# Kernel tuning notes

Measured on AMD Instinct MI355X. Metric: run time of the kernel, lower is better.

## Reference

```python
import jax, jax.numpy as jnp
import numpy as np

N = 2048          # num atoms
ATOM_D = 64       # atom embedding dim
H = 8             # num heads
NB = 8            # num bond types
D = ATOM_D * H    # 512, Q/K/V output dim
NEG_SLOPE = 0.2


def setup_inputs() -> dict:
    key = jax.random.key(0)
    ks = jax.random.split(key, 12)
    inp = {
        "atom_embeddings": jax.random.normal(ks[0], (N, ATOM_D), dtype=jnp.float32),
        # bond type per (i, j); -1 means no bond (masked)
        "edges": jax.random.randint(ks[1], (N, N), -1, NB, dtype=jnp.int32),
        "Qw": jax.random.normal(ks[2], (ATOM_D, D), dtype=jnp.float32) / np.sqrt(ATOM_D),
        "Qb": jnp.zeros((D,), dtype=jnp.float32),
        "Kw": jax.random.normal(ks[3], (ATOM_D, D), dtype=jnp.float32) / np.sqrt(ATOM_D),
        "Kb": jnp.zeros((D,), dtype=jnp.float32),
        "Vw": jax.random.normal(ks[4], (ATOM_D, D), dtype=jnp.float32) / np.sqrt(ATOM_D),
        "Vb": jnp.zeros((D,), dtype=jnp.float32),
        # per-bond-type attention weights: (NB, 2*D, H), xavier-ish scale
        "a": jax.random.normal(ks[5], (NB, 2 * D, H), dtype=jnp.float32) * np.sqrt(2.0 / (2 * D + H)) * 1.414,
        "Pw": jax.random.normal(ks[6], (D, ATOM_D), dtype=jnp.float32) / np.sqrt(D),
        "Pb": jnp.zeros((ATOM_D,), dtype=jnp.float32),
    }
    return inp


def reference(atom_embeddings, edges, Qw, Qb, Kw, Kb, Vw, Vb, a, Pw, Pb):
    n, d = atom_embeddings.shape
    nb, two_d, h = a.shape
    D_ = two_d // 2
    Q = atom_embeddings @ Qw + Qb          # (N, D)
    K = atom_embeddings @ Kw + Kb          # (N, D)
    V = atom_embeddings @ Vw + Vb          # (N, D)

    # a[k] applies to concat(Q_i, K_j): split into src / dst halves
    A1 = a[:, :D_, :]                      # (NB, D, H)
    A2 = a[:, D_:, :]                      # (NB, D, H)
    # precompute per-node, per-bond-type partial scores (avoids the dense
    # one-hot scatter of the original: direct per-edge-type weight indexing)
    S1 = jnp.einsum('id,kdh->ikh', Q, A1)  # (N, NB, H)
    S2 = jnp.einsum('jd,kdh->jkh', K, A2)  # (N, NB, H)

    kidx = jnp.clip(edges, 0, nb - 1)      # (N, N)
    rows = jnp.arange(n)
    # e[i,j,h] = S1[i, edges[i,j], h] + S2[j, edges[i,j], h]
    e = S1[rows[:, None], kidx] + S2[rows[None, :], kidx]   # (N, N, H)
    valid = (edges >= 0)[..., None]
    # masked edges get all-zero rows in the original scatter -> score exactly 0
    e = jnp.where(valid, jax.nn.leaky_relu(e, negative_slope=NEG_SLOPE), 0.0)

    attn = jax.nn.softmax(e, axis=1)       # softmax over neighbor j
    Vh = V.reshape(n, h, d)                # (N, H, atom_d)
    out = jnp.einsum('ijh,jhd->ihd', attn, Vh).reshape(n, h * d)
    return out @ Pw + Pb                   # (N, atom_d)
```

## Files before the change

kernel.cpp:

```cpp
#include <hip/hip_runtime.h>

#define NN 2048
#define AD 64
#define HH 8
#define DD 512
#define NEG 0.2f

typedef float f32x4 __attribute__((ext_vector_type(4)));
typedef _Float16 half8 __attribute__((ext_vector_type(8)));
typedef _Float16 half2v __attribute__((ext_vector_type(2)));
typedef unsigned short u16;
typedef unsigned int u32;
typedef u16 u16x8 __attribute__((ext_vector_type(8)));

__global__ __launch_bounds__(256) void prep_vth_kernel(
    const float* __restrict__ Qw, const float* __restrict__ Qb,
    const float* __restrict__ Kw, const float* __restrict__ Kb,
    const float* __restrict__ A,
    const float* __restrict__ X,
    const float* __restrict__ Vw, const float* __restrict__ Vb,
    float* __restrict__ W1, float* __restrict__ W2, float* __restrict__ c12,
    u16* __restrict__ VtH) {
  __shared__ float As[512][8];
  __shared__ float Ws8[8][516];
  __shared__ float red[4][8][8];
  __shared__ float red2[8][8];
  __shared__ float Xs[64][68];
  int t = threadIdx.x;
  int b = blockIdx.x;
  if (b < 128) {
    int mat = b >> 6;
    int k = (b >> 3) & 7;
    int dg = b & 7;
    int d0 = dg * 8;
    const float* Asrc = A + (size_t)k * 8192 + mat * 4096;
    const float* Wsrc = (mat ? Kw : Qw) + (size_t)d0 * DD;

    float* Asf = &As[0][0];
    for (int idx = t; idx < 4096; idx += 256) Asf[idx] = Asrc[idx];
    for (int idx = t; idx < 4096; idx += 256) {
      int dd = idx >> 9, c = idx & 511;
      Ws8[dd][c] = Wsrc[idx];
    }
    __syncthreads();

    int dd = t & 7, h = (t >> 3) & 7, cs = t >> 6;
    int cbase = cs * 128;
    float acc = 0.f;
#pragma unroll 4
    for (int c = 0; c < 128; ++c) {
      acc += Ws8[dd][cbase + c] * As[cbase + c][h];
    }
    red[cs][dd][h] = acc;
    __syncthreads();
    if (t < 64) {
      int dd2 = t >> 3, h2 = t & 7;
      float v = red[0][dd2][h2] + red[1][dd2][h2] + red[2][dd2][h2] + red[3][dd2][h2];
      (mat ? W2 : W1)[(d0 + dd2) * 64 + k * 8 + h2] = v;
    }
    if (dg == 0) {
      if (t < 64) {
        int h2 = t >> 3, seg = t & 7;
        const float* bs = mat ? Kb : Qb;
        float a2 = 0.f;
        for (int i = 0; i < 64; ++i) {
          int c = seg * 64 + i;
          a2 += bs[c] * As[c][h2];
        }
        red2[h2][seg] = a2;
      }
      __syncthreads();
      if (t < 8) {
        float s = 0.f;
#pragma unroll
        for (int seg = 0; seg < 8; ++seg) s += red2[t][seg];
        c12[mat * 64 + k * 8 + t] = s;
      }
    }
  } else {
    int tile = b - 128;
    int r0 = (tile >> 2) * 64;
    int d0 = (tile & 3) * 128;

    for (int idx = t; idx < 64 * 64; idx += 256) {
      int r = idx >> 6, c = idx & 63;
      Xs[r][c] = X[(size_t)(r0 + r) * AD + c];
    }
    __syncthreads();

    int tr = t >> 5;
    int td = t & 31;
    int d = d0 + td * 4;
    float4 bias = *(const float4*)&Vb[d];
    float4 acc[8];
#pragma unroll
    for (int i = 0; i < 8; ++i) acc[i] = bias;
    for (int c = 0; c < 64; ++c) {
      float4 w = *(const float4*)&Vw[c * DD + d];
#pragma unroll
      for (int i = 0; i < 8; ++i) {
        float x = Xs[tr * 8 + i][c];
        acc[i].x += x * w.x; acc[i].y += x * w.y;
        acc[i].z += x * w.z; acc[i].w += x * w.w;
      }
    }
#pragma unroll
    for (int c = 0; c < 4; ++c) {
      u16x8 o;
#pragma unroll
      for (int i = 0; i < 8; ++i) {
        float fv = (c == 0) ? acc[i].x : (c == 1) ? acc[i].y
                 : (c == 2) ? acc[i].z : acc[i].w;
        _Float16 hf = (_Float16)fv;
        o[i] = __builtin_bit_cast(u16, hf);
      }
      *(u16x8*)&VtH[(size_t)(d + c) * NN + r0 + tr * 8] = o;
    }
  }
}

__global__ __launch_bounds__(256) void stab_kernel(
    const float* __restrict__ X,
    const float* __restrict__ W1, const float* __restrict__ W2,
    const float* __restrict__ c12,
    u16* __restrict__ TS1, u16* __restrict__ TS2) {
  __shared__ float W1L[64][65];
  __shared__ float W2L[64][65];
  __shared__ float XS[16][65];
  __shared__ __align__(16) u16 T1S[16][128];
  __shared__ __align__(16) u16 T2S[16][128];
  int t = threadIdx.x;
  int r0 = blockIdx.x * 16;
  for (int i = t; i < 4096; i += 256) {
    int d = i >> 6, kh = i & 63;
    W1L[d][kh] = W1[i];
    W2L[d][kh] = W2[i];
  }
  {
    int r = t >> 4, c = (t & 15) * 4;
    float4 xv = *(const float4*)&X[(size_t)(r0 + r) * AD + c];
    XS[r][c] = xv.x; XS[r][c + 1] = xv.y; XS[r][c + 2] = xv.z; XS[r][c + 3] = xv.w;
  }
  __syncthreads();
  int r = t >> 4, khq = t & 15;
  float a1[4], a2[4];
#pragma unroll
  for (int i = 0; i < 4; ++i) {
    a1[i] = c12[khq * 4 + i];
    a2[i] = c12[64 + khq * 4 + i];
  }
  for (int d = 0; d < 64; ++d) {
    float x = XS[r][d];
#pragma unroll
    for (int i = 0; i < 4; ++i) {
      a1[i] += x * W1L[d][khq * 4 + i];
      a2[i] += x * W2L[d][khq * 4 + i];
    }
  }
#pragma unroll
  for (int i = 0; i < 4; ++i) {
    int kh = khq * 4 + i, k = kh >> 3, h = kh & 7;
    int kki = (k ^ (r & 7)) << 4;
    _Float16 p1 = (_Float16)(__expf(a1[i]) * 0.25f);
    _Float16 n1 = (_Float16)(__expf(NEG * a1[i]) * 0.25f);
    _Float16 p2 = (_Float16)(__expf(a2[i]) * 0.25f);
    _Float16 n2 = (_Float16)(__expf(NEG * a2[i]) * 0.25f);
    T1S[r][kki + h]     = __builtin_bit_cast(u16, p1);
    T1S[r][kki + 8 + h] = __builtin_bit_cast(u16, n1);
    T2S[r][kki + h]     = __builtin_bit_cast(u16, p2);
    T2S[r][kki + 8 + h] = __builtin_bit_cast(u16, n2);
  }
  __syncthreads();
  {
    const u16* s1 = &T1S[0][0];
    const u16* s2 = &T2S[0][0];
    *(u16x8*)&TS1[(size_t)r0 * 128 + t * 8] = *(const u16x8*)&s1[t * 8];
    *(u16x8*)&TS2[(size_t)r0 * 128 + t * 8] = *(const u16x8*)&s2[t * 8];
  }
}

__global__ __launch_bounds__(512, 4) void attn_mfma_kernel(
    const int* __restrict__ E,
    const u16* __restrict__ TS1, const u16* __restrict__ TS2,
    const u16* __restrict__ VtH,
    float* __restrict__ PART, float* __restrict__ LPART) {
  __shared__ _Float16 s1t[16 * 128];
  __shared__ _Float16 s2t[2][64 * 128];
  __shared__ _Float16 PA[2][8][16][72];
  int t = threadIdx.x;
  int w = t >> 6, lane = t & 63;
  int li = lane & 15, q = lane >> 4;
  int m = lane & 31;
  int i_loc = w * 2 + (lane >> 5);
  int it = blockIdx.x >> 1, ch = blockIdx.x & 1;
  int i0 = it * 16, jch = ch * 1024;

  const half8 SIX8 = {(_Float16)0.0625f, (_Float16)0.0625f, (_Float16)0.0625f,
                      (_Float16)0.0625f, (_Float16)0.0625f, (_Float16)0.0625f,
                      (_Float16)0.0625f, (_Float16)0.0625f};
  const half8 ONE8 = {(_Float16)1.0f, (_Float16)1.0f, (_Float16)1.0f,
                      (_Float16)1.0f, (_Float16)1.0f, (_Float16)1.0f,
                      (_Float16)1.0f, (_Float16)1.0f};

  if (t < 256) {
    *(u16x8*)&s1t[t * 8] = *(const u16x8*)&TS1[(size_t)i0 * 128 + t * 8];
  }
  {
    const u16* src = TS2 + (size_t)jch * 128;
    *(u16x8*)&s2t[0][t * 8]        = *(const u16x8*)&src[t * 8];
    *(u16x8*)&s2t[0][4096 + t * 8] = *(const u16x8*)&src[4096 + t * 8];
  }
  u16x8 stA = *(const u16x8*)&TS2[(size_t)(jch + 64) * 128 + t * 8];
  u16x8 stB = *(const u16x8*)&TS2[(size_t)(jch + 64) * 128 + 4096 + t * 8];
  const int* Erow = E + (size_t)(i0 + i_loc) * NN;
  int2 eCur = *(const int2*)(Erow + jch + 2 * m);
  int2 eNxt = *(const int2*)(Erow + jch + 64 + 2 * m);
  __syncthreads();

  f32x4 acc[4];
#pragma unroll
  for (int n = 0; n < 4; ++n) acc[n] = (f32x4){0.f, 0.f, 0.f, 0.f};
  f32x4 acc_l = (f32x4){0.f, 0.f, 0.f, 0.f};
  int cur = 0;

#pragma unroll 1
  for (int jt = 0; jt < 16; ++jt) {
    int jb = jch + jt * 64;

    u16x8 stA2, stB2;
    int2 eN2 = eNxt;
    if (jt < 14) {
      const u16* src = TS2 + (size_t)(jb + 128) * 128;
      stA2 = *(const u16x8*)&src[t * 8];
      stB2 = *(const u16x8*)&src[4096 + t * 8];
      eN2 = *(const int2*)(Erow + jb + 128 + 2 * m);
    }

    half8 bfrag[4][2];
#pragma unroll
    for (int n = 0; n < 4; ++n)
#pragma unroll
      for (int s = 0; s < 2; ++s) {
        const u16* p = &VtH[(size_t)(w * 64 + n * 16 + li) * NN + jb + s * 32 + q * 8];
        bfrag[n][s] = *(const half8*)p;
      }

    const _Float16* s1row = &s1t[i_loc * 128];
    const _Float16* s2row = &s2t[cur][0];
    half8 pmj[2];
#pragma unroll
    for (int jj = 0; jj < 2; ++jj) {
      int ev = jj ? eCur.y : eCur.x;
      int j = 2 * m + jj;
      int k = min(max(ev, 0), 7);
      int kki = (k ^ (i_loc & 7)) << 4;
      int kkj = (k ^ (j & 7)) << 4;
      half8 ip = *(const half8*)&s1row[kki];
      half8 in_ = *(const half8*)&s1row[kki + 8];
      half8 jp = *(const half8*)&s2row[j * 128 + kkj];
      half8 jn = *(const half8*)&s2row[j * 128 + kkj + 8];
      half8 pp = ip * jp;
      half8 pn = in_ * jn;
      half8 pm = __builtin_elementwise_max(pp, pn);
      if (ev < 0) pm = SIX8;
      pmj[jj] = pm;
    }
#pragma unroll
    for (int h = 0; h < 8; ++h) {
      half2v wv = {pmj[0][h], pmj[1][h]};
      *(half2v*)&PA[cur][h][i_loc][2 * m] = wv;
    }

    if (jt < 15) {
      *(u16x8*)&s2t[cur ^ 1][t * 8]        = stA;
      *(u16x8*)&s2t[cur ^ 1][4096 + t * 8] = stB;
    }

    asm volatile("s_waitcnt lgkmcnt(0)" ::: "memory");
    __builtin_amdgcn_s_barrier();

    half8 af0 = *(const half8*)&PA[cur][w][li][q * 8];
    half8 af1 = *(const half8*)&PA[cur][w][li][32 + q * 8];
    __builtin_amdgcn_s_setprio(1);
#pragma unroll
    for (int n = 0; n < 4; ++n) {
      acc[n] = __builtin_amdgcn_mfma_f32_16x16x32_f16(af0, bfrag[n][0], acc[n], 0, 0, 0);
      acc[n] = __builtin_amdgcn_mfma_f32_16x16x32_f16(af1, bfrag[n][1], acc[n], 0, 0, 0);
    }
    acc_l = __builtin_amdgcn_mfma_f32_16x16x32_f16(af0, ONE8, acc_l, 0, 0, 0);
    acc_l = __builtin_amdgcn_mfma_f32_16x16x32_f16(af1, ONE8, acc_l, 0, 0, 0);
    __builtin_amdgcn_s_setprio(0);

    stA = stA2; stB = stB2;
    eCur = eNxt; eNxt = eN2;
    cur ^= 1;
  }

  if (li == 0) {
#pragma unroll
    for (int r = 0; r < 4; ++r)
      LPART[((size_t)ch * NN + i0 + q * 4 + r) * 8 + w] = acc_l[r];
  }

  float* base = PART + (size_t)ch * NN * DD;
#pragma unroll
  for (int n = 0; n < 4; ++n) {
#pragma unroll
    for (int r = 0; r < 4; ++r) {
      int row = i0 + q * 4 + r;
      int col = w * 64 + n * 16 + li;
      base[(size_t)row * DD + col] = acc[n][r];
    }
  }
}

__global__ __launch_bounds__(256) void proj_kernel(
    const float* __restrict__ PART, const float* __restrict__ LPART,
    const float* __restrict__ Pw, const float* __restrict__ Pb,
    float* __restrict__ out) {
  __shared__ __align__(16) float preS[4][512];
  __shared__ float linv[4][8];
  int t = threadIdx.x;
  int r0 = blockIdx.x * 4;
  if (t < 32) {
    int i = t >> 3, h = t & 7;
    float s = 0.f;
#pragma unroll
    for (int c = 0; c < 2; ++c)
      s += LPART[(size_t)c * NN * 8 + (size_t)(r0 + i) * 8 + h];
    linv[i][h] = 1.0f / s;
  }
  __syncthreads();
  for (int idx = t; idx < 4 * 128; idx += 256) {
    int i = idx >> 7, hd = (idx & 127) * 4;
    float4 v = {0.f, 0.f, 0.f, 0.f};
#pragma unroll
    for (int c = 0; c < 2; ++c) {
      float4 p = *(const float4*)&PART[(size_t)c * NN * DD + (size_t)(r0 + i) * DD + hd];
      v.x += p.x; v.y += p.y; v.z += p.z; v.w += p.w;
    }
    float li2 = linv[i][hd >> 6];
    v.x *= li2; v.y *= li2; v.z *= li2; v.w *= li2;
    *(float4*)&preS[i][hd] = v;
  }
  __syncthreads();
  int c = t & 63, rq = t >> 6;
  float acc0 = Pb[c];
  for (int hq = 0; hq < 128; ++hq) {
    int hd = hq * 4;
    float4 p0 = *(const float4*)&preS[rq][hd];
    float w0 = Pw[(hd + 0) * 64 + c];
    float w1 = Pw[(hd + 1) * 64 + c];
    float w2 = Pw[(hd + 2) * 64 + c];
    float w3 = Pw[(hd + 3) * 64 + c];
    acc0 += p0.x * w0 + p0.y * w1 + p0.z * w2 + p0.w * w3;
  }
  out[(size_t)(r0 + rq) * 64 + c] = acc0;
}

extern "C" void kernel_launch(void* const* d_in, const int* in_sizes, int n_in,
                              void* d_out, int out_size, void* d_ws, size_t ws_size,
                              hipStream_t stream) {
  const float* X  = (const float*)d_in[0];
  const int*   E  = (const int*)d_in[1];
  const float* Qw = (const float*)d_in[2];
  const float* Qb = (const float*)d_in[3];
  const float* Kw = (const float*)d_in[4];
  const float* Kb = (const float*)d_in[5];
  const float* Vw = (const float*)d_in[6];
  const float* Vb = (const float*)d_in[7];
  const float* A  = (const float*)d_in[8];
  const float* Pw = (const float*)d_in[9];
  const float* Pb = (const float*)d_in[10];
  float* out = (float*)d_out;

  float* ws = (float*)d_ws;
  const size_t ND = (size_t)NN * DD;
  float* PART  = ws;
  u16*   TS1   = (u16*)(ws + 2 * ND);
  u16*   TS2   = TS1 + (size_t)NN * 128;
  u16*   VtH   = TS2 + (size_t)NN * 128;
  float* LPART = (float*)(VtH + (size_t)DD * NN);
  float* W1    = LPART + (size_t)2 * NN * 8;
  float* W2    = W1 + 4096;
  float* c12   = W2 + 4096;

  prep_vth_kernel<<<256, 256, 0, stream>>>(Qw, Qb, Kw, Kb, A, X, Vw, Vb,
                                           W1, W2, c12, VtH);
  stab_kernel<<<128, 256, 0, stream>>>(X, W1, W2, c12, TS1, TS2);
  attn_mfma_kernel<<<256, 512, 0, stream>>>(E, TS1, TS2, VtH, PART, LPART);
  proj_kernel<<<512, 256, 0, stream>>>(PART, LPART, Pw, Pb, out);
}
```

Measured before the change: 66.92 us.

## Fuse four kernels into one cooperative kernel with grid-wide syncs

Merges the prep/V-projection, score-table, attention MFMA and output-projection kernels into a single cooperative launch of 256 blocks of 512 threads, separated by grid.sync() barriers. Each phase's thread mapping is adapted to 512 threads and shared memory is carved from one buffer. This removes three kernel launch boundaries and their drain/fill gaps. In exchange, grid barriers add their own cost, the projection phase now runs on half as many blocks, and the attention phase drops from four to two blocks per CU by launch bounds.

```diff
diff --git a/kernel.cpp b/kernel.cpp
--- a/kernel.cpp
+++ b/kernel.cpp
@@ -1,4 +1,7 @@
 #include <hip/hip_runtime.h>
+#include <hip/hip_cooperative_groups.h>
+
+namespace cg = cooperative_groups;
 
 #define NN 2048
 #define AD 64
@@ -12,22 +15,24 @@
 typedef unsigned short u16;
 typedef unsigned int u32;
 typedef u16 u16x8 __attribute__((ext_vector_type(8)));
-
-__global__ __launch_bounds__(256) void prep_vth_kernel(
+typedef u16 u16x4 __attribute__((ext_vector_type(4)));
+
+__global__ __launch_bounds__(512, 2) void fused_kernel(
     const float* __restrict__ Qw, const float* __restrict__ Qb,
     const float* __restrict__ Kw, const float* __restrict__ Kb,
-    const float* __restrict__ A,
-    const float* __restrict__ X,
+    const float* __restrict__ A,  const float* __restrict__ X,
     const float* __restrict__ Vw, const float* __restrict__ Vb,
+    const int* __restrict__ E,
+    const float* __restrict__ Pw, const float* __restrict__ Pb,
     float* __restrict__ W1, float* __restrict__ W2, float* __restrict__ c12,
-    u16* __restrict__ VtH) {
-  __shared__ float As[512][8];
-  __shared__ float Ws8[8][516];
-  __shared__ float red[4][8][8];
-  __shared__ float red2[8][8];
-  __shared__ float Xs[64][68];
+    u16* __restrict__ VtH, u16* __restrict__ TS1, u16* __restrict__ TS2,
+    float* __restrict__ PART, float* __restrict__ LPART,
+    float* __restrict__ out) {
+  __shared__ __align__(16) char smem[73728];
+  cg::grid_group grid = cg::this_grid();
   int t = threadIdx.x;
   int b = blockIdx.x;
+
   if (b < 128) {
     int mat = b >> 6;
     int k = (b >> 3) & 7;
@@ -35,327 +40,314 @@
     int d0 = dg * 8;
     const float* Asrc = A + (size_t)k * 8192 + mat * 4096;
     const float* Wsrc = (mat ? Kw : Qw) + (size_t)d0 * DD;
-
-    float* Asf = &As[0][0];
-    for (int idx = t; idx < 4096; idx += 256) Asf[idx] = Asrc[idx];
-    for (int idx = t; idx < 4096; idx += 256) {
+    float* As  = (float*)smem;
+    float* Ws8 = (float*)(smem + 16384);
+    float* red = (float*)(smem + 32896);
+    float* red2= (float*)(smem + 34944);
+
+    for (int idx = t; idx < 4096; idx += 512) As[idx] = Asrc[idx];
+    for (int idx = t; idx < 4096; idx += 512) {
       int dd = idx >> 9, c = idx & 511;
-      Ws8[dd][c] = Wsrc[idx];
+      Ws8[dd * 516 + c] = Wsrc[idx];
     }
     __syncthreads();
 
     int dd = t & 7, h = (t >> 3) & 7, cs = t >> 6;
-    int cbase = cs * 128;
+    int cbase = cs * 64;
     float acc = 0.f;
 #pragma unroll 4
-    for (int c = 0; c < 128; ++c) {
-      acc += Ws8[dd][cbase + c] * As[cbase + c][h];
-    }
-    red[cs][dd][h] = acc;
+    for (int c = 0; c < 64; ++c) {
+      acc += Ws8[dd * 516 + cbase + c] * As[(cbase + c) * 8 + h];
+    }
+    red[(cs * 8 + dd) * 8 + h] = acc;
     __syncthreads();
     if (t < 64) {
       int dd2 = t >> 3, h2 = t & 7;
-      float v = red[0][dd2][h2] + red[1][dd2][h2] + red[2][dd2][h2] + red[3][dd2][h2];
+      float v = 0.f;
+#pragma unroll
+      for (int c2 = 0; c2 < 8; ++c2) v += red[(c2 * 8 + dd2) * 8 + h2];
       (mat ? W2 : W1)[(d0 + dd2) * 64 + k * 8 + h2] = v;
     }
-    if (dg == 0) {
-      if (t < 64) {
-        int h2 = t >> 3, seg = t & 7;
-        const float* bs = mat ? Kb : Qb;
-        float a2 = 0.f;
-        for (int i = 0; i < 64; ++i) {
-          int c = seg * 64 + i;
-          a2 += bs[c] * As[c][h2];
-        }
-        red2[h2][seg] = a2;
-      }
-      __syncthreads();
-      if (t < 8) {
-        float s = 0.f;
-#pragma unroll
-        for (int seg = 0; seg < 8; ++seg) s += red2[t][seg];
-        c12[mat * 64 + k * 8 + t] = s;
-      }
+    if (dg == 0 && t < 64) {
+      int h2 = t >> 3, seg = t & 7;
+      const float* bs = mat ? Kb : Qb;
+      float a2 = 0.f;
+      for (int i = 0; i < 64; ++i) {
+        int c = seg * 64 + i;
+        a2 += bs[c] * As[c * 8 + h2];
+      }
+      red2[h2 * 8 + seg] = a2;
+    }
+    __syncthreads();
+    if (dg == 0 && t < 8) {
+      float s = 0.f;
+#pragma unroll
+      for (int seg = 0; seg < 8; ++seg) s += red2[t * 8 + seg];
+      c12[mat * 64 + k * 8 + t] = s;
     }
   } else {
     int tile = b - 128;
     int r0 = (tile >> 2) * 64;
     int d0 = (tile & 3) * 128;
-
-    for (int idx = t; idx < 64 * 64; idx += 256) {
+    float* Xs = (float*)smem;
+
+    for (int idx = t; idx < 4096; idx += 512) {
       int r = idx >> 6, c = idx & 63;
-      Xs[r][c] = X[(size_t)(r0 + r) * AD + c];
-    }
-    __syncthreads();
-
-    int tr = t >> 5;
-    int td = t & 31;
-    int d = d0 + td * 4;
-    float4 bias = *(const float4*)&Vb[d];
-    float4 acc[8];
+      Xs[r * 68 + c] = X[(size_t)(r0 + r) * AD + c];
+    }
+    __syncthreads();
+
+    int tr = t >> 6;
+    int td = t & 63;
+    int d = d0 + td * 2;
+    float2 bias = *(const float2*)&Vb[d];
+    float2 acc[8];
 #pragma unroll
     for (int i = 0; i < 8; ++i) acc[i] = bias;
     for (int c = 0; c < 64; ++c) {
-      float4 w = *(const float4*)&Vw[c * DD + d];
+      float2 wv = *(const float2*)&Vw[c * DD + d];
 #pragma unroll
       for (int i = 0; i < 8; ++i) {
-        float x = Xs[tr * 8 + i][c];
-        acc[i].x += x * w.x; acc[i].y += x * w.y;
-        acc[i].z += x * w.z; acc[i].w += x * w.w;
-      }
-    }
-#pragma unroll
-    for (int c = 0; c < 4; ++c) {
+        float x = Xs[(tr * 8 + i) * 68 + c];
+        acc[i].x += x * wv.x; acc[i].y += x * wv.y;
+      }
+    }
+#pragma unroll
+    for (int cc = 0; cc < 2; ++cc) {
       u16x8 o;
 #pragma unroll
       for (int i = 0; i < 8; ++i) {
-        float fv = (c == 0) ? acc[i].x : (c == 1) ? acc[i].y
-                 : (c == 2) ? acc[i].z : acc[i].w;
+        float fv = cc ? acc[i].y : acc[i].x;
         _Float16 hf = (_Float16)fv;
         o[i] = __builtin_bit_cast(u16, hf);
       }
-      *(u16x8*)&VtH[(size_t)(d + c) * NN + r0 + tr * 8] = o;
+      *(u16x8*)&VtH[(size_t)(d + cc) * NN + r0 + tr * 8] = o;
     }
   }
-}
-
-__global__ __launch_bounds__(256) void stab_kernel(
-    const float* __restrict__ X,
-    const float* __restrict__ W1, const float* __restrict__ W2,
-    const float* __restrict__ c12,
-    u16* __restrict__ TS1, u16* __restrict__ TS2) {
-  __shared__ float W1L[64][65];
-  __shared__ float W2L[64][65];
-  __shared__ float XS[16][65];
-  __shared__ __align__(16) u16 T1S[16][128];
-  __shared__ __align__(16) u16 T2S[16][128];
-  int t = threadIdx.x;
-  int r0 = blockIdx.x * 16;
-  for (int i = t; i < 4096; i += 256) {
-    int d = i >> 6, kh = i & 63;
-    W1L[d][kh] = W1[i];
-    W2L[d][kh] = W2[i];
+
+  grid.sync();
+
+  if (b < 128) {
+    float* W1L = (float*)smem;
+    float* W2L = (float*)(smem + 16640);
+    float* XS  = (float*)(smem + 33280);
+    u16* T1S   = (u16*)(smem + 37440);
+    u16* T2S   = (u16*)(smem + 41536);
+    int r0 = b * 16;
+    for (int i = t; i < 4096; i += 512) {
+      int d = i >> 6, kh = i & 63;
+      W1L[d * 65 + kh] = W1[i];
+      W2L[d * 65 + kh] = W2[i];
+    }
+    {
+      int r = t >> 5, c = (t & 31) * 2;
+      float2 xv = *(const float2*)&X[(size_t)(r0 + r) * AD + c];
+      XS[r * 65 + c] = xv.x; XS[r * 65 + c + 1] = xv.y;
+    }
+    __syncthreads();
+    int r = t >> 5, khq = t & 31;
+    float a1[2], a2[2];
+#pragma unroll
+    for (int i = 0; i < 2; ++i) {
+      a1[i] = c12[khq * 2 + i];
+      a2[i] = c12[64 + khq * 2 + i];
+    }
+    for (int d = 0; d < 64; ++d) {
+      float x = XS[r * 65 + d];
+#pragma unroll
+      for (int i = 0; i < 2; ++i) {
+        a1[i] += x * W1L[d * 65 + khq * 2 + i];
+        a2[i] += x * W2L[d * 65 + khq * 2 + i];
+      }
+    }
+#pragma unroll
+    for (int i = 0; i < 2; ++i) {
+      int kh = khq * 2 + i, k = kh >> 3, h = kh & 7;
+      int kki = (k ^ (r & 7)) << 4;
+      _Float16 p1 = (_Float16)(__expf(a1[i]) * 0.25f);
+      _Float16 n1 = (_Float16)(__expf(NEG * a1[i]) * 0.25f);
+      _Float16 p2 = (_Float16)(__expf(a2[i]) * 0.25f);
+      _Float16 n2 = (_Float16)(__expf(NEG * a2[i]) * 0.25f);
+      T1S[r * 128 + kki + h]     = __builtin_bit_cast(u16, p1);
+      T1S[r * 128 + kki + 8 + h] = __builtin_bit_cast(u16, n1);
+      T2S[r * 128 + kki + h]     = __builtin_bit_cast(u16, p2);
+      T2S[r * 128 + kki + 8 + h] = __builtin_bit_cast(u16, n2);
+    }
+    __syncthreads();
+    *(u16x4*)&TS1[(size_t)r0 * 128 + t * 4] = *(const u16x4*)&T1S[t * 4];
+    *(u16x4*)&TS2[(size_t)r0 * 128 + t * 4] = *(const u16x4*)&T2S[t * 4];
   }
+
+  grid.sync();
+
   {
-    int r = t >> 4, c = (t & 15) * 4;
-    float4 xv = *(const float4*)&X[(size_t)(r0 + r) * AD + c];
-    XS[r][c] = xv.x; XS[r][c + 1] = xv.y; XS[r][c + 2] = xv.z; XS[r][c + 3] = xv.w;
+    _Float16* s1t = (_Float16*)smem;
+    _Float16* s2t = (_Float16*)(smem + 4096);
+    _Float16* PAb = (_Float16*)(smem + 36864);
+    int w = t >> 6, lane = t & 63;
+    int li = lane & 15, q = lane >> 4;
+    int m = lane & 31;
+    int i_loc = w * 2 + (lane >> 5);
+    int it = b >> 1, ch = b & 1;
+    int i0 = it * 16, jch = ch * 1024;
+
+    const half8 SIX8 = {(_Float16)0.0625f, (_Float16)0.0625f, (_Float16)0.0625f,
+                        (_Float16)0.0625f, (_Float16)0.0625f, (_Float16)0.0625f,
+                        (_Float16)0.0625f, (_Float16)0.0625f};
+    const half8 ONE8 = {(_Float16)1.0f, (_Float16)1.0f, (_Float16)1.0f,
+                        (_Float16)1.0f, (_Float16)1.0f, (_Float16)1.0f,
+                        (_Float16)1.0f, (_Float16)1.0f};
+
+    if (t < 256) {
+      *(u16x8*)&s1t[t * 8] = *(const u16x8*)&TS1[(size_t)i0 * 128 + t * 8];
+    }
+    {
+      const u16* src = TS2 + (size_t)jch * 128;
+      *(u16x8*)&s2t[t * 8]        = *(const u16x8*)&src[t * 8];
+      *(u16x8*)&s2t[4096 + t * 8] = *(const u16x8*)&src[4096 + t * 8];
+    }
+    u16x8 stA = *(const u16x8*)&TS2[(size_t)(jch + 64) * 128 + t * 8];
+    u16x8 stB = *(const u16x8*)&TS2[(size_t)(jch + 64) * 128 + 4096 + t * 8];
+    const int* Erow = E + (size_t)(i0 + i_loc) * NN;
+    int2 eCur = *(const int2*)(Erow + jch + 2 * m);
+    int2 eNxt = *(const int2*)(Erow + jch + 64 + 2 * m);
+    __syncthreads();
+
+    f32x4 acc[4];
+#pragma unroll
+    for (int n = 0; n < 4; ++n) acc[n] = (f32x4){0.f, 0.f, 0.f, 0.f};
+    f32x4 acc_l = (f32x4){0.f, 0.f, 0.f, 0.f};
+    int cur = 0;
+
+#pragma unroll 1
+    for (int jt = 0; jt < 16; ++jt) {
+      int jb = jch + jt * 64;
+
+      u16x8 stA2, stB2;
+      int2 eN2 = eNxt;
+      if (jt < 14) {
+        const u16* src = TS2 + (size_t)(jb + 128) * 128;
+        stA2 = *(const u16x8*)&src[t * 8];
+        stB2 = *(const u16x8*)&src[4096 + t * 8];
+        eN2 = *(const int2*)(Erow + jb + 128 + 2 * m);
+      }
+
+      half8 bfrag[4][2];
+#pragma unroll
+      for (int n = 0; n < 4; ++n)
+#pragma unroll
+        for (int s = 0; s < 2; ++s) {
+          const u16* p = &VtH[(size_t)(w * 64 + n * 16 + li) * NN + jb + s * 32 + q * 8];
+          bfrag[n][s] = *(const half8*)p;
+        }
+
+      const _Float16* s1row = &s1t[i_loc * 128];
+      const _Float16* s2row = &s2t[cur * 8192];
+      half8 pmj[2];
+#pragma unroll
+      for (int jj = 0; jj < 2; ++jj) {
+        int ev = jj ? eCur.y : eCur.x;
+        int j = 2 * m + jj;
+        int k = min(max(ev, 0), 7);
+        int kki = (k ^ (i_loc & 7)) << 4;
+        int kkj = (k ^ (j & 7)) << 4;
+        half8 ip = *(const half8*)&s1row[kki];
+        half8 in_ = *(const half8*)&s1row[kki + 8];
+        half8 jp = *(const half8*)&s2row[j * 128 + kkj];
+        half8 jn = *(const half8*)&s2row[j * 128 + kkj + 8];
+        half8 pp = ip * jp;
+        half8 pn = in_ * jn;
+        half8 pm = __builtin_elementwise_max(pp, pn);
+        if (ev < 0) pm = SIX8;
+        pmj[jj] = pm;
+      }
+#pragma unroll
+      for (int h = 0; h < 8; ++h) {
+        half2v wv = {pmj[0][h], pmj[1][h]};
+        *(half2v*)&PAb[((cur * 8 + h) * 16 + i_loc) * 72 + 2 * m] = wv;
+      }
+
+      if (jt < 15) {
+        *(u16x8*)&s2t[(cur ^ 1) * 8192 + t * 8]        = stA;
+        *(u16x8*)&s2t[(cur ^ 1) * 8192 + 4096 + t * 8] = stB;
+      }
+
+      asm volatile("s_waitcnt lgkmcnt(0)" ::: "memory");
+      __builtin_amdgcn_s_barrier();
+
+      half8 af0 = *(const half8*)&PAb[((cur * 8 + w) * 16 + li) * 72 + q * 8];
+      half8 af1 = *(const half8*)&PAb[((cur * 8 + w) * 16 + li) * 72 + 32 + q * 8];
+      __builtin_amdgcn_s_setprio(1);
+#pragma unroll
+      for (int n = 0; n < 4; ++n) {
+        acc[n] = __builtin_amdgcn_mfma_f32_16x16x32_f16(af0, bfrag[n][0], acc[n], 0, 0, 0);
+        acc[n] = __builtin_amdgcn_mfma_f32_16x16x32_f16(af1, bfrag[n][1], acc[n], 0, 0, 0);
+      }
+      acc_l = __builtin_amdgcn_mfma_f32_16x16x32_f16(af0, ONE8, acc_l, 0, 0, 0);
+      acc_l = __builtin_amdgcn_mfma_f32_16x16x32_f16(af1, ONE8, acc_l, 0, 0, 0);
+      __builtin_amdgcn_s_setprio(0);
+
+      stA = stA2; stB = stB2;
+      eCur = eNxt; eNxt = eN2;
+      cur ^= 1;
+    }
+
+    if (li == 0) {
+#pragma unroll
+      for (int r = 0; r < 4; ++r)
+        LPART[((size_t)ch * NN + i0 + q * 4 + r) * 8 + w] = acc_l[r];
+    }
+    float* base = PART + (size_t)ch * NN * DD;
+#pragma unroll
+    for (int n = 0; n < 4; ++n) {
+#pragma unroll
+      for (int r = 0; r < 4; ++r) {
+        int row = i0 + q * 4 + r;
+        int col = w * 64 + n * 16 + li;
+        base[(size_t)row * DD + col] = acc[n][r];
+      }
+    }
   }
-  __syncthreads();
-  int r = t >> 4, khq = t & 15;
-  float a1[4], a2[4];
-#pragma unroll
-  for (int i = 0; i < 4; ++i) {
-    a1[i] = c12[khq * 4 + i];
-    a2[i] = c12[64 + khq * 4 + i];
+
+  grid.sync();
+
+  {
+    float* preS = (float*)smem;
+    float* linv = (float*)(smem + 16384);
+    int r0 = b * 8;
+    if (t < 64) {
+      int i = t >> 3, h = t & 7;
+      float s = LPART[(size_t)(r0 + i) * 8 + h] +
+                LPART[(size_t)NN * 8 + (size_t)(r0 + i) * 8 + h];
+      linv[i * 8 + h] = 1.0f / s;
+    }
+    __syncthreads();
+    for (int idx = t; idx < 8 * 128; idx += 512) {
+      int i = idx >> 7, hd = (idx & 127) * 4;
+      float4 v = {0.f, 0.f, 0.f, 0.f};
+#pragma unroll
+      for (int c = 0; c < 2; ++c) {
+        float4 p = *(const float4*)&PART[(size_t)c * NN * DD + (size_t)(r0 + i) * DD + hd];
+        v.x += p.x; v.y += p.y; v.z += p.z; v.w += p.w;
+      }
+      float li2 = linv[i * 8 + (hd >> 6)];
+      v.x *= li2; v.y *= li2; v.z *= li2; v.w *= li2;
+      *(float4*)&preS[i * 512 + hd] = v;
+    }
+    __syncthreads();
+    int c = t & 63, rq = t >> 6;
+    float acc0 = Pb[c];
+    for (int hq = 0; hq < 128; ++hq) {
+      int hd = hq * 4;
+      float4 p0 = *(const float4*)&preS[rq * 512 + hd];
+      float w0 = Pw[(hd + 0) * 64 + c];
+      float w1 = Pw[(hd + 1) * 64 + c];
+      float w2 = Pw[(hd + 2) * 64 + c];
+      float w3 = Pw[(hd + 3) * 64 + c];
+      acc0 += p0.x * w0 + p0.y * w1 + p0.z * w2 + p0.w * w3;
+    }
+    out[(size_t)(r0 + rq) * 64 + c] = acc0;
   }
-  for (int d = 0; d < 64; ++d) {
-    float x = XS[r][d];
-#pragma unroll
-    for (int i = 0; i < 4; ++i) {
-      a1[i] += x * W1L[d][khq * 4 + i];
-      a2[i] += x * W2L[d][khq * 4 + i];
-    }
-  }
-#pragma unroll
-  for (int i = 0; i < 4; ++i) {
-    int kh = khq * 4 + i, k = kh >> 3, h = kh & 7;
-    int kki = (k ^ (r & 7)) << 4;
-    _Float16 p1 = (_Float16)(__expf(a1[i]) * 0.25f);
-    _Float16 n1 = (_Float16)(__expf(NEG * a1[i]) * 0.25f);
-    _Float16 p2 = (_Float16)(__expf(a2[i]) * 0.25f);
-    _Float16 n2 = (_Float16)(__expf(NEG * a2[i]) * 0.25f);
-    T1S[r][kki + h]     = __builtin_bit_cast(u16, p1);
-    T1S[r][kki + 8 + h] = __builtin_bit_cast(u16, n1);
-    T2S[r][kki + h]     = __builtin_bit_cast(u16, p2);
-    T2S[r][kki + 8 + h] = __builtin_bit_cast(u16, n2);
-  }
-  __syncthreads();
-  {
-    const u16* s1 = &T1S[0][0];
-    const u16* s2 = &T2S[0][0];
-    *(u16x8*)&TS1[(size_t)r0 * 128 + t * 8] = *(const u16x8*)&s1[t * 8];
-    *(u16x8*)&TS2[(size_t)r0 * 128 + t * 8] = *(const u16x8*)&s2[t * 8];
-  }
-}
-
-__global__ __launch_bounds__(512, 4) void attn_mfma_kernel(
-    const int* __restrict__ E,
-    const u16* __restrict__ TS1, const u16* __restrict__ TS2,
-    const u16* __restrict__ VtH,
-    float* __restrict__ PART, float* __restrict__ LPART) {
-  __shared__ _Float16 s1t[16 * 128];
-  __shared__ _Float16 s2t[2][64 * 128];
-  __shared__ _Float16 PA[2][8][16][72];
-  int t = threadIdx.x;
-  int w = t >> 6, lane = t & 63;
-  int li = lane & 15, q = lane >> 4;
-  int m = lane & 31;
-  int i_loc = w * 2 + (lane >> 5);
-  int it = blockIdx.x >> 1, ch = blockIdx.x & 1;
-  int i0 = it * 16, jch = ch * 1024;
-
-  const half8 SIX8 = {(_Float16)0.0625f, (_Float16)0.0625f, (_Float16)0.0625f,
-                      (_Float16)0.0625f, (_Float16)0.0625f, (_Float16)0.0625f,
-                      (_Float16)0.0625f, (_Float16)0.0625f};
-  const half8 ONE8 = {(_Float16)1.0f, (_Float16)1.0f, (_Float16)1.0f,
-                      (_Float16)1.0f, (_Float16)1.0f, (_Float16)1.0f,
-                      (_Float16)1.0f, (_Float16)1.0f};
-
-  if (t < 256) {
-    *(u16x8*)&s1t[t * 8] = *(const u16x8*)&TS1[(size_t)i0 * 128 + t * 8];
-  }
-  {
-    const u16* src = TS2 + (size_t)jch * 128;
-    *(u16x8*)&s2t[0][t * 8]        = *(const u16x8*)&src[t * 8];
-    *(u16x8*)&s2t[0][4096 + t * 8] = *(const u16x8*)&src[4096 + t * 8];
-  }
-  u16x8 stA = *(const u16x8*)&TS2[(size_t)(jch + 64) * 128 + t * 8];
-  u16x8 stB = *(const u16x8*)&TS2[(size_t)(jch + 64) * 128 + 4096 + t * 8];
-  const int* Erow = E + (size_t)(i0 + i_loc) * NN;
-  int2 eCur = *(const int2*)(Erow + jch + 2 * m);
-  int2 eNxt = *(const int2*)(Erow + jch + 64 + 2 * m);
-  __syncthreads();
-
-  f32x4 acc[4];
-#pragma unroll
-  for (int n = 0; n < 4; ++n) acc[n] = (f32x4){0.f, 0.f, 0.f, 0.f};
-  f32x4 acc_l = (f32x4){0.f, 0.f, 0.f, 0.f};
-  int cur = 0;
-
-#pragma unroll 1
-  for (int jt = 0; jt < 16; ++jt) {
-    int jb = jch + jt * 64;
-
-    u16x8 stA2, stB2;
-    int2 eN2 = eNxt;
-    if (jt < 14) {
-      const u16* src = TS2 + (size_t)(jb + 128) * 128;
-      stA2 = *(const u16x8*)&src[t * 8];
-      stB2 = *(const u16x8*)&src[4096 + t * 8];
-      eN2 = *(const int2*)(Erow + jb + 128 + 2 * m);
-    }
-
-    half8 bfrag[4][2];
-#pragma unroll
-    for (int n = 0; n < 4; ++n)
-#pragma unroll
-      for (int s = 0; s < 2; ++s) {
-        const u16* p = &VtH[(size_t)(w * 64 + n * 16 + li) * NN + jb + s * 32 + q * 8];
-        bfrag[n][s] = *(const half8*)p;
-      }
-
-    const _Float16* s1row = &s1t[i_loc * 128];
-    const _Float16* s2row = &s2t[cur][0];
-    half8 pmj[2];
-#pragma unroll
-    for (int jj = 0; jj < 2; ++jj) {
-      int ev = jj ? eCur.y : eCur.x;
-      int j = 2 * m + jj;
-      int k = min(max(ev, 0), 7);
-      int kki = (k ^ (i_loc & 7)) << 4;
-      int kkj = (k ^ (j & 7)) << 4;
-      half8 ip = *(const half8*)&s1row[kki];
-      half8 in_ = *(const half8*)&s1row[kki + 8];
-      half8 jp = *(const half8*)&s2row[j * 128 + kkj];
-      half8 jn = *(const half8*)&s2row[j * 128 + kkj + 8];
-      half8 pp = ip * jp;
-      half8 pn = in_ * jn;
-      half8 pm = __builtin_elementwise_max(pp, pn);
-      if (ev < 0) pm = SIX8;
-      pmj[jj] = pm;
-    }
-#pragma unroll
-    for (int h = 0; h < 8; ++h) {
-      half2v wv = {pmj[0][h], pmj[1][h]};
-      *(half2v*)&PA[cur][h][i_loc][2 * m] = wv;
-    }
-
-    if (jt < 15) {
-      *(u16x8*)&s2t[cur ^ 1][t * 8]        = stA;
-      *(u16x8*)&s2t[cur ^ 1][4096 + t * 8] = stB;
-    }
-
-    asm volatile("s_waitcnt lgkmcnt(0)" ::: "memory");
-    __builtin_amdgcn_s_barrier();
-
-    half8 af0 = *(const half8*)&PA[cur][w][li][q * 8];
-    half8 af1 = *(const half8*)&PA[cur][w][li][32 + q * 8];
-    __builtin_amdgcn_s_setprio(1);
-#pragma unroll
-    for (int n = 0; n < 4; ++n) {
-      acc[n] = __builtin_amdgcn_mfma_f32_16x16x32_f16(af0, bfrag[n][0], acc[n], 0, 0, 0);
-      acc[n] = __builtin_amdgcn_mfma_f32_16x16x32_f16(af1, bfrag[n][1], acc[n], 0, 0, 0);
-    }
-    acc_l = __builtin_amdgcn_mfma_f32_16x16x32_f16(af0, ONE8, acc_l, 0, 0, 0);
-    acc_l = __builtin_amdgcn_mfma_f32_16x16x32_f16(af1, ONE8, acc_l, 0, 0, 0);
-    __builtin_amdgcn_s_setprio(0);
-
-    stA = stA2; stB = stB2;
-    eCur = eNxt; eNxt = eN2;
-    cur ^= 1;
-  }
-
-  if (li == 0) {
-#pragma unroll
-    for (int r = 0; r < 4; ++r)
-      LPART[((size_t)ch * NN + i0 + q * 4 + r) * 8 + w] = acc_l[r];
-  }
-
-  float* base = PART + (size_t)ch * NN * DD;
-#pragma unroll
-  for (int n = 0; n < 4; ++n) {
-#pragma unroll
-    for (int r = 0; r < 4; ++r) {
-      int row = i0 + q * 4 + r;
-      int col = w * 64 + n * 16 + li;
-      base[(size_t)row * DD + col] = acc[n][r];
-    }
-  }
-}
-
-__global__ __launch_bounds__(256) void proj_kernel(
-    const float* __restrict__ PART, const float* __restrict__ LPART,
-    const float* __restrict__ Pw, const float* __restrict__ Pb,
-    float* __restrict__ out) {
-  __shared__ __align__(16) float preS[4][512];
-  __shared__ float linv[4][8];
-  int t = threadIdx.x;
-  int r0 = blockIdx.x * 4;
-  if (t < 32) {
-    int i = t >> 3, h = t & 7;
-    float s = 0.f;
-#pragma unroll
-    for (int c = 0; c < 2; ++c)
-      s += LPART[(size_t)c * NN * 8 + (size_t)(r0 + i) * 8 + h];
-    linv[i][h] = 1.0f / s;
-  }
-  __syncthreads();
-  for (int idx = t; idx < 4 * 128; idx += 256) {
-    int i = idx >> 7, hd = (idx & 127) * 4;
-    float4 v = {0.f, 0.f, 0.f, 0.f};
-#pragma unroll
-    for (int c = 0; c < 2; ++c) {
-      float4 p = *(const float4*)&PART[(size_t)c * NN * DD + (size_t)(r0 + i) * DD + hd];
-      v.x += p.x; v.y += p.y; v.z += p.z; v.w += p.w;
-    }
-    float li2 = linv[i][hd >> 6];
-    v.x *= li2; v.y *= li2; v.z *= li2; v.w *= li2;
-    *(float4*)&preS[i][hd] = v;
-  }
-  __syncthreads();
-  int c = t & 63, rq = t >> 6;
-  float acc0 = Pb[c];
-  for (int hq = 0; hq < 128; ++hq) {
-    int hd = hq * 4;
-    float4 p0 = *(const float4*)&preS[rq][hd];
-    float w0 = Pw[(hd + 0) * 64 + c];
-    float w1 = Pw[(hd + 1) * 64 + c];
-    float w2 = Pw[(hd + 2) * 64 + c];
-    float w3 = Pw[(hd + 3) * 64 + c];
-    acc0 += p0.x * w0 + p0.y * w1 + p0.z * w2 + p0.w * w3;
-  }
-  out[(size_t)(r0 + rq) * 64 + c] = acc0;
 }
 
 extern "C" void kernel_launch(void* const* d_in, const int* in_sizes, int n_in,
@@ -385,9 +377,12 @@
   float* W2    = W1 + 4096;
   float* c12   = W2 + 4096;
 
-  prep_vth_kernel<<<256, 256, 0, stream>>>(Qw, Qb, Kw, Kb, A, X, Vw, Vb,
-                                           W1, W2, c12, VtH);
-  stab_kernel<<<128, 256, 0, stream>>>(X, W1, W2, c12, TS1, TS2);
-  attn_mfma_kernel<<<256, 512, 0, stream>>>(E, TS1, TS2, VtH, PART, LPART);
-  proj_kernel<<<512, 256, 0, stream>>>(PART, LPART, Pw, Pb, out);
+  void* args[] = {
+    (void*)&Qw, (void*)&Qb, (void*)&Kw, (void*)&Kb, (void*)&A, (void*)&X,
+    (void*)&Vw, (void*)&Vb, (void*)&E, (void*)&Pw, (void*)&Pb,
+    (void*)&W1, (void*)&W2, (void*)&c12, (void*)&VtH, (void*)&TS1,
+    (void*)&TS2, (void*)&PART, (void*)&LPART, (void*)&out
+  };
+  hipLaunchCooperativeKernel((void*)fused_kernel, dim3(256), dim3(512),
+                             args, 0, stream);
 }
```

After: 168.2 us. 2.51x slower.

## Fuse projection into attention kernel via last-block-done atomic counter

Applied to the files above, without the earlier changes.

Removes the separate proj_kernel launch. Each attention block fences its partial outputs and increments a per-row-tile counter. The second of the two j-chunk blocks to finish combines PART and LPART, normalizes, and applies the Pw projection, reusing shared memory. The counters are zeroed in the prep kernel. This saves a kernel launch and an extra pass over PART, at the cost of atomics, fences, and a serial tail on half the blocks.

```diff
diff --git a/kernel.cpp b/kernel.cpp
--- a/kernel.cpp
+++ b/kernel.cpp
@@ -20,7 +20,7 @@
     const float* __restrict__ X,
     const float* __restrict__ Vw, const float* __restrict__ Vb,
     float* __restrict__ W1, float* __restrict__ W2, float* __restrict__ c12,
-    u16* __restrict__ VtH) {
+    u16* __restrict__ VtH, int* __restrict__ flags) {
   __shared__ float As[512][8];
   __shared__ float Ws8[8][516];
   __shared__ float red[4][8][8];
@@ -78,6 +78,7 @@
       }
     }
   } else {
+    if (b == 128 && t < 128) flags[t] = 0;
     int tile = b - 128;
     int r0 = (tile >> 2) * 64;
     int d0 = (tile & 3) * 128;
@@ -183,10 +184,13 @@
     const int* __restrict__ E,
     const u16* __restrict__ TS1, const u16* __restrict__ TS2,
     const u16* __restrict__ VtH,
-    float* __restrict__ PART, float* __restrict__ LPART) {
+    const float* __restrict__ Pw, const float* __restrict__ Pb,
+    float* __restrict__ PART, float* __restrict__ LPART,
+    int* __restrict__ flags, float* __restrict__ out) {
   __shared__ _Float16 s1t[16 * 128];
   __shared__ _Float16 s2t[2][64 * 128];
   __shared__ _Float16 PA[2][8][16][72];
+  __shared__ int sflag;
   int t = threadIdx.x;
   int w = t >> 6, lane = t & 63;
   int li = lane & 15, q = lane >> 4;
@@ -312,50 +316,48 @@
       base[(size_t)row * DD + col] = acc[n][r];
     }
   }
-}
-
-__global__ __launch_bounds__(256) void proj_kernel(
-    const float* __restrict__ PART, const float* __restrict__ LPART,
-    const float* __restrict__ Pw, const float* __restrict__ Pb,
-    float* __restrict__ out) {
-  __shared__ __align__(16) float preS[4][512];
-  __shared__ float linv[4][8];
-  int t = threadIdx.x;
-  int r0 = blockIdx.x * 4;
-  if (t < 32) {
-    int i = t >> 3, h = t & 7;
-    float s = 0.f;
-#pragma unroll
-    for (int c = 0; c < 2; ++c)
-      s += LPART[(size_t)c * NN * 8 + (size_t)(r0 + i) * 8 + h];
-    linv[i][h] = 1.0f / s;
-  }
+
+  __threadfence();
+  if (t == 0) sflag = atomicAdd(&flags[it], 1);
   __syncthreads();
-  for (int idx = t; idx < 4 * 128; idx += 256) {
-    int i = idx >> 7, hd = (idx & 127) * 4;
-    float4 v = {0.f, 0.f, 0.f, 0.f};
-#pragma unroll
-    for (int c = 0; c < 2; ++c) {
-      float4 p = *(const float4*)&PART[(size_t)c * NN * DD + (size_t)(r0 + i) * DD + hd];
-      v.x += p.x; v.y += p.y; v.z += p.z; v.w += p.w;
-    }
-    float li2 = linv[i][hd >> 6];
-    v.x *= li2; v.y *= li2; v.z *= li2; v.w *= li2;
-    *(float4*)&preS[i][hd] = v;
-  }
-  __syncthreads();
-  int c = t & 63, rq = t >> 6;
-  float acc0 = Pb[c];
-  for (int hq = 0; hq < 128; ++hq) {
-    int hd = hq * 4;
-    float4 p0 = *(const float4*)&preS[rq][hd];
-    float w0 = Pw[(hd + 0) * 64 + c];
-    float w1 = Pw[(hd + 1) * 64 + c];
-    float w2 = Pw[(hd + 2) * 64 + c];
-    float w3 = Pw[(hd + 3) * 64 + c];
-    acc0 += p0.x * w0 + p0.y * w1 + p0.z * w2 + p0.w * w3;
-  }
-  out[(size_t)(r0 + rq) * 64 + c] = acc0;
+  if (sflag == 1) {
+    __threadfence();
+    float* preS = (float*)&s2t[0][0];
+    float* linv = (float*)&s1t[0];
+    if (t < 128) {
+      int i = t >> 3, h = t & 7;
+      float s = LPART[(size_t)(i0 + i) * 8 + h] +
+                LPART[(size_t)NN * 8 + (size_t)(i0 + i) * 8 + h];
+      linv[i * 8 + h] = 1.0f / s;
+    }
+    __syncthreads();
+    for (int idx = t; idx < 16 * 128; idx += 512) {
+      int i = idx >> 7, hd = (idx & 127) * 4;
+      float4 p0 = *(const float4*)&PART[(size_t)(i0 + i) * DD + hd];
+      float4 p1 = *(const float4*)&PART[(size_t)NN * DD + (size_t)(i0 + i) * DD + hd];
+      float li2 = linv[i * 8 + (hd >> 6)];
+      float4 v;
+      v.x = (p0.x + p1.x) * li2; v.y = (p0.y + p1.y) * li2;
+      v.z = (p0.z + p1.z) * li2; v.w = (p0.w + p1.w) * li2;
+      *(float4*)&preS[i * 512 + hd] = v;
+    }
+    __syncthreads();
+    int c = t & 63, rq = t >> 6;
+    float acc0 = Pb[c], acc1 = Pb[c];
+    for (int hq = 0; hq < 128; ++hq) {
+      int hd = hq * 4;
+      float4 pa = *(const float4*)&preS[rq * 512 + hd];
+      float4 pb = *(const float4*)&preS[(rq + 8) * 512 + hd];
+      float w0 = Pw[(hd + 0) * 64 + c];
+      float w1 = Pw[(hd + 1) * 64 + c];
+      float w2 = Pw[(hd + 2) * 64 + c];
+      float w3 = Pw[(hd + 3) * 64 + c];
+      acc0 += pa.x * w0 + pa.y * w1 + pa.z * w2 + pa.w * w3;
+      acc1 += pb.x * w0 + pb.y * w1 + pb.z * w2 + pb.w * w3;
+    }
+    out[(size_t)(i0 + rq) * 64 + c] = acc0;
+    out[(size_t)(i0 + rq + 8) * 64 + c] = acc1;
+  }
 }
 
 extern "C" void kernel_launch(void* const* d_in, const int* in_sizes, int n_in,
@@ -384,10 +386,11 @@
   float* W1    = LPART + (size_t)2 * NN * 8;
   float* W2    = W1 + 4096;
   float* c12   = W2 + 4096;
+  int*   flags = (int*)(c12 + 128);
 
   prep_vth_kernel<<<256, 256, 0, stream>>>(Qw, Qb, Kw, Kb, A, X, Vw, Vb,
-                                           W1, W2, c12, VtH);
+                                           W1, W2, c12, VtH, flags);
   stab_kernel<<<128, 256, 0, stream>>>(X, W1, W2, c12, TS1, TS2);
-  attn_mfma_kernel<<<256, 512, 0, stream>>>(E, TS1, TS2, VtH, PART, LPART);
-  proj_kernel<<<512, 256, 0, stream>>>(PART, LPART, Pw, Pb, out);
+  attn_mfma_kernel<<<256, 512, 0, stream>>>(E, TS1, TS2, VtH, Pw, Pb,
+                                            PART, LPART, flags, out);
 }
```

Result: slower. 154.0 us (+130.1%).
